# Kernel tuning notes

Hardware: AMD Instinct MI355X
Metric: run time of the kernel (lower is better)

## Reference

```python
import jax, jax.numpy as jnp
import numpy as np

K_SIM_SCHEDULE = [4, 8, 16]
K_CON_SCHEDULE = [2, 4, 8]
NEG = 1000000000.0


def _dual_adjacency(h, k_sim, k_con):
    """Binary causal dual adjacency (similar / dissimilar), no gradient."""
    B, T, D = h.shape
    h = jax.lax.stop_gradient(h)
    xn = h / jnp.maximum(jnp.linalg.norm(h, axis=-1, keepdims=True), 1e-12)
    sim = jnp.einsum('btd,bsd->bts', xn, xn)                 # (B,T,T)
    past = jnp.tril(jnp.ones((T, T), h.dtype), -1)           # strictly-past mask
    sim = sim * past - NEG * (1.0 - past)
    eff_sim = min(k_sim, T - 1)
    eff_con = min(k_con, max(0, T - 1 - eff_sim))
    bI = jnp.arange(B)[:, None, None]
    tI = jnp.arange(T)[None, :, None]
    A_sim = jnp.zeros((B, T, T), h.dtype)
    if eff_sim > 0:
        _, top_idx = jax.lax.top_k(sim, eff_sim)             # (B,T,k)
        A_sim = A_sim.at[bI, tI, top_idx].set(1.0) * past
    A_con = jnp.zeros((B, T, T), h.dtype)
    if eff_con > 0:
        sim_con = jnp.where(A_sim > 0, NEG, sim)
        _, bot_idx = jax.lax.top_k(-sim_con, eff_con)        # smallest eff_con
        A_con = A_con.at[bI, tI, bot_idx].set(1.0) * past * (1.0 - A_sim)
    return A_sim, A_con


def _aggregate(h, A):
    # unweighted mean over selected neighbors; empty rows -> zeros
    deg = jnp.sum(A, axis=-1, keepdims=True)
    return jnp.einsum('bts,bsd->btd', A, h) / jnp.maximum(deg, 1.0)


def setup_inputs() -> dict:
    key = jax.random.key(0)
    ks = jax.random.split(key, 2)
    B, T, D, R = 4, 2048, 512, 3
    x = jax.random.normal(ks[0], (B, T, D), dtype=jnp.float32)
    gain = jnp.ones((R, D), dtype=jnp.float32)
    bias = jnp.zeros((R, D), dtype=jnp.float32)
    log_mix = jnp.zeros((R,), dtype=jnp.float32)
    log_alpha = jnp.zeros((R,), dtype=jnp.float32)
    log_momentum = jnp.asarray(1.0, dtype=jnp.float32)
    log_scale = jnp.asarray(0.0, dtype=jnp.float32)
    return {"x": x, "gain": gain, "bias": bias, "log_mix": log_mix,
            "log_alpha": log_alpha, "log_momentum": log_momentum,
            "log_scale": log_scale}


def reference(x, gain, bias, log_mix, log_alpha, log_momentum, log_scale):
    momentum = jax.nn.sigmoid(log_momentum)
    scale = jax.nn.softplus(log_scale) + 0.01
    h = x
    for r in range(len(K_SIM_SCHEDULE)):
        mix = jax.nn.sigmoid(log_mix[r])
        alpha = jax.nn.sigmoid(log_alpha[r])
        A_sim, A_con = _dual_adjacency(h, K_SIM_SCHEDULE[r], K_CON_SCHEDULE[r])
        msg_pos = _aggregate(h, A_sim)
        msg_neg = _aggregate(h, A_con)
        ctx = alpha * msg_pos + (1.0 - alpha) * msg_neg
        blended = mix * h + (1.0 - mix) * ctx
        h_new = jax.nn.gelu(blended * gain[r] + bias[r], approximate=False)
        h = momentum * h + (1.0 - momentum) * h_new
    return (h - x) * scale
```

## Files before the change

### kernel.cpp

```cpp
#include <hip/hip_runtime.h>
#include <hip/hip_bf16.h>
#include <cstdint>
#include <cstddef>

#define BB 4
#define TT 2048
#define DD 512
#define NEG_INF (-3.402823466e+38f)
#define POS_INF (3.402823466e+38f)

typedef __attribute__((ext_vector_type(8))) short bf16x8;
typedef __attribute__((ext_vector_type(8))) unsigned short ushort8;
typedef __attribute__((ext_vector_type(4))) float f32x4;

__device__ __forceinline__ float sigmoidf_(float x){ return 1.0f/(1.0f+expf(-x)); }

__device__ __forceinline__ unsigned short f2bf(float x){
  __hip_bfloat16 b = __float2bfloat16(x);
  return *reinterpret_cast<unsigned short*>(&b);
}

__device__ __forceinline__ unsigned int fwd_map(float f){
  unsigned int b = __float_as_uint(f);
  return b ^ ((b & 0x80000000u) ? 0xFFFFFFFFu : 0x80000000u);
}
__device__ __forceinline__ float inv_map(unsigned int u){
  unsigned int b = (u & 0x80000000u) ? (u ^ 0x80000000u) : ~u;
  return __uint_as_float(b);
}

__device__ __forceinline__ unsigned long long shfl_xor64(unsigned long long x, int off){
  unsigned int hi = __shfl_xor((unsigned int)(x >> 32), off);
  unsigned int lo = __shfl_xor((unsigned int)x, off);
  return ((unsigned long long)hi << 32) | lo;
}

__global__ __launch_bounds__(64) void k_normsplit(const float* __restrict__ h, float* __restrict__ rnorm,
                                                  unsigned short* __restrict__ Xh, unsigned short* __restrict__ Xl){
  int row = blockIdx.x;
  const float* hr = h + (size_t)row*DD;
  int lane = threadIdx.x;
  float4 v0 = *(const float4*)&hr[lane*4];
  float4 v1 = *(const float4*)&hr[lane*4 + 256];
  float ss = v0.x*v0.x+v0.y*v0.y+v0.z*v0.z+v0.w*v0.w
           + v1.x*v1.x+v1.y*v1.y+v1.z*v1.z+v1.w*v1.w;
  #pragma unroll
  for (int off=32; off; off>>=1) ss += __shfl_xor(ss, off);
  float rn = 1.0f / fmaxf(sqrtf(ss), 1e-12f);
  if (lane==0) rnorm[row] = rn;

  float xs[8] = {v0.x,v0.y,v0.z,v0.w,v1.x,v1.y,v1.z,v1.w};
  unsigned short hb[8], lb[8];
  #pragma unroll
  for (int q=0;q<8;q++){
    float xn = xs[q]*rn;
    unsigned short hh = f2bf(xn);
    __hip_bfloat16 bh = *reinterpret_cast<__hip_bfloat16*>(&hh);
    float rem = xn - __bfloat162float(bh);
    hb[q] = hh; lb[q] = f2bf(rem);
  }
  ushort4 h0 = {hb[0],hb[1],hb[2],hb[3]}, h1 = {hb[4],hb[5],hb[6],hb[7]};
  ushort4 l0 = {lb[0],lb[1],lb[2],lb[3]}, l1 = {lb[4],lb[5],lb[6],lb[7]};
  *(ushort4*)&Xh[(size_t)row*DD + lane*4]       = h0;
  *(ushort4*)&Xh[(size_t)row*DD + lane*4 + 256] = h1;
  *(ushort4*)&Xl[(size_t)row*DD + lane*4]       = l0;
  *(ushort4*)&Xl[(size_t)row*DD + lane*4 + 256] = l1;
}

__global__ __launch_bounds__(256) void k_sim(const unsigned short* __restrict__ Xh,
                                             const unsigned short* __restrict__ Xl,
                                             float* __restrict__ sim, int b0){
  int p = blockIdx.x;
  int jt = (int)((sqrtf(8.0f*(float)p + 1.0f) - 1.0f)*0.5f);
  while ((jt+1)*(jt+2)/2 <= p) jt++;
  while (jt*(jt+1)/2 > p) jt--;
  int is = p - jt*(jt+1)/2;

  int bl = blockIdx.y;
  size_t xoff = (size_t)(b0 + bl)*TT*DD;
  const unsigned short* XhB = Xh + xoff;
  const unsigned short* XlB = Xl + xoff;
  float* simb = sim + (size_t)bl*TT*TT;
  int t0 = jt*128, s0 = is*128;

  __shared__ __align__(16) short As[128*32];
  __shared__ __align__(16) short Bs[128*32];

  int tid = threadIdx.x, wave = tid>>6, lane = tid&63;
  int wr = wave>>1, wc = wave&1;

  int srow = tid>>2;
  int sc8  = (tid&3)*8;

  f32x4 acc[4][4];
  #pragma unroll
  for (int m=0;m<4;m++)
    #pragma unroll
    for (int n=0;n<4;n++) acc[m][n] = (f32x4){0.f,0.f,0.f,0.f};

  ushort8 ra0, ra1, rb0, rb1;
  auto gload = [&](int s){
    int pass = s>>4; int kcol = (s&15)*32;
    const unsigned short* sA = (pass<2) ? XhB : XlB;
    const unsigned short* sB = (pass!=1) ? XhB : XlB;
    ra0 = *(const ushort8*)&sA[(size_t)(t0+srow)*DD + kcol + sc8];
    ra1 = *(const ushort8*)&sA[(size_t)(t0+srow+64)*DD + kcol + sc8];
    rb0 = *(const ushort8*)&sB[(size_t)(s0+srow)*DD + kcol + sc8];
    rb1 = *(const ushort8*)&sB[(size_t)(s0+srow+64)*DD + kcol + sc8];
  };

  gload(0);
  for (int s=0; s<48; ++s){
    __syncthreads();
    *(ushort8*)&As[srow*32 + sc8]      = ra0;
    *(ushort8*)&As[(srow+64)*32 + sc8] = ra1;
    *(ushort8*)&Bs[srow*32 + sc8]      = rb0;
    *(ushort8*)&Bs[(srow+64)*32 + sc8] = rb1;
    __syncthreads();
    if (s < 47) gload(s+1);

    int arow = wr*64 + (lane&15);
    int brow = wc*64 + (lane&15);
    int kb = (lane>>4)*8;
    bf16x8 af[4], bf[4];
    #pragma unroll
    for (int m=0;m<4;m++) af[m] = *(const bf16x8*)&As[(arow + m*16)*32 + kb];
    #pragma unroll
    for (int n=0;n<4;n++) bf[n] = *(const bf16x8*)&Bs[(brow + n*16)*32 + kb];
    #pragma unroll
    for (int m=0;m<4;m++)
      #pragma unroll
      for (int n=0;n<4;n++)
        acc[m][n] = __builtin_amdgcn_mfma_f32_16x16x32_bf16(af[m], bf[n], acc[m][n], 0, 0, 0);
  }

  #pragma unroll
  for (int m=0;m<4;m++){
    int t = t0 + wr*64 + m*16 + (lane>>4)*4;
    #pragma unroll
    for (int n=0;n<4;n++){
      int sc = s0 + wc*64 + n*16 + (lane&15);
      float* dst = simb + (size_t)t*TT + sc;
      #pragma unroll
      for (int j=0;j<4;j++) dst[(size_t)j*TT] = acc[m][n][j];
    }
  }
}

#define BMASK 0xFFFFFF00u
#define MKKEY(F,S) ((((unsigned long long)fwd_map(F)) << 32) | (unsigned int)(~(S)))
#define INS(KK) do{ unsigned long long a=(KK); \
  if (a > kv3){ \
    if (a > kv0){ unsigned long long tq=kv0; kv0=a; a=tq; } \
    if (a > kv1){ unsigned long long tq=kv1; kv1=a; a=tq; } \
    if (a > kv2){ unsigned long long tq=kv2; kv2=a; a=tq; } \
    kv3=a; } }while(0)

__device__ __forceinline__ unsigned int radix24(const float* __restrict__ srow, int t, int k1,
                                                unsigned int flip, int* sh, int lane){
  #pragma unroll
  for (int i=0;i<4;i++) sh[lane + i*64] = 0;
  int t4 = t & ~3;
  for (int s4 = lane*4; s4 < t4; s4 += 256){
    float4 f = *(const float4*)&srow[s4];
    unsigned int u0=fwd_map(f.x)^flip, u1=fwd_map(f.y)^flip, u2=fwd_map(f.z)^flip, u3=fwd_map(f.w)^flip;
    atomicAdd(&sh[u0>>24],1); atomicAdd(&sh[u1>>24],1);
    atomicAdd(&sh[u2>>24],1); atomicAdd(&sh[u3>>24],1);
  }
  for (int s = t4 + lane; s < t; s += 64){
    unsigned int u = fwd_map(srow[s])^flip;
    atomicAdd(&sh[u>>24],1);
  }
  unsigned int pfx = 0u; int kp = k1;
  #pragma unroll
  for (int pass = 0; pass < 3; ++pass){
    int shift = 24 - 8*pass;
    int m4 = sh[4*lane] + sh[4*lane+1] + sh[4*lane+2] + sh[4*lane+3];
    int x = __shfl(m4, 63-lane);
    #pragma unroll
    for (int off = 1; off < 64; off <<= 1){
      int v = __shfl_up(x, off);
      if (lane >= off) x += v;
    }
    int T = __shfl(x, 63-lane);
    int G = T - m4;
    bool hit = (G < kp) && (kp <= T);
    unsigned int npfx = 0u; int nkp = 0;
    if (hit){
      int c = G; int D = 4*lane;
      #pragma unroll
      for (int i = 3; i >= 0; --i){
        int hc = sh[4*lane + i];
        if (kp <= c + hc){ D = 4*lane + i; break; }
        c += hc;
      }
      npfx = pfx | ((unsigned int)D << shift);
      nkp = kp - c;
    }
    unsigned long long hm = __ballot(hit);
    int src = __ffsll(hm) - 1;
    pfx = __shfl(npfx, src);
    kp  = __shfl(nkp, src);
    if (pass == 2) break;

    int nshift = shift - 8;
    unsigned int keep = 0xFFFFFFFFu << shift;
    #pragma unroll
    for (int i=0;i<4;i++) sh[lane + i*64] = 0;
    for (int s4 = lane*4; s4 < t4; s4 += 256){
      float4 f = *(const float4*)&srow[s4];
      unsigned int u0=fwd_map(f.x)^flip, u1=fwd_map(f.y)^flip, u2=fwd_map(f.z)^flip, u3=fwd_map(f.w)^flip;
      if (((u0 ^ pfx) & keep) == 0) atomicAdd(&sh[(u0>>nshift)&255],1);
      if (((u1 ^ pfx) & keep) == 0) atomicAdd(&sh[(u1>>nshift)&255],1);
      if (((u2 ^ pfx) & keep) == 0) atomicAdd(&sh[(u2>>nshift)&255],1);
      if (((u3 ^ pfx) & keep) == 0) atomicAdd(&sh[(u3>>nshift)&255],1);
    }
    for (int s = t4 + lane; s < t; s += 64){
      unsigned int u = fwd_map(srow[s])^flip;
      if (((u ^ pfx) & keep) == 0) atomicAdd(&sh[(u>>nshift)&255],1);
    }
  }
  return pfx;
}

template<int ESIM, int ECON>
__global__ __launch_bounds__(256) void k_topk(const float* __restrict__ sim, int b0,
                                              const float* __restrict__ h, const float* __restrict__ rnorm,
                                              int* __restrict__ topidx, int* __restrict__ botidx,
                                              int* __restrict__ bcnt){
  constexpr int K1  = ESIM + 8;
  constexpr int K1B = ESIM + ECON + 8;
  constexpr int CANDCAP = 40;
  constexpr int EQCAP = 44;
  constexpr float TAU = 5e-5f;
  __shared__ int s_hist[4][256];
  __shared__ int s_cand[4][CANDCAP];
  __shared__ int s_eq[4][EQCAP];
  __shared__ int s_sel[4][ESIM];
  __shared__ int s_bot[4][16];
  __shared__ int s_cnt[4][2];

  int tid = threadIdx.x, lane = tid & 63, wid = tid >> 6;
  int lrow = blockIdx.x*4 + wid;
  int bl = lrow >> 11, t = lrow & (TT-1);
  int gb = b0 + bl;
  int grow = (gb << 11) | t;

  if (t <= ESIM){
    if (lane < t) topidx[(size_t)grow*16 + lane] = lane;
    if (lane == 0) bcnt[grow] = 0;
    return;
  }
  const float* srow = sim + (size_t)lrow*TT;
  const float* hb  = h + (size_t)gb*TT*DD;
  const float* rnb = rnorm + (size_t)gb*TT;

  int* sh    = s_hist[wid];
  int* scand = s_cand[wid];
  int* seq   = s_eq[wid];
  int* ssel  = s_sel[wid];
  int* sbot  = s_bot[wid];
  int t4 = t & ~3;

  unsigned long long kv0=0, kv1=0, kv2=0, kv3=0;
  {
    int s4 = lane*4;
    for (; s4 + 772 <= t4; s4 += 1024){
      float4 f0 = *(const float4*)&srow[s4];
      float4 f1 = *(const float4*)&srow[s4+256];
      float4 f2 = *(const float4*)&srow[s4+512];
      float4 f3 = *(const float4*)&srow[s4+768];
      INS(MKKEY(f0.x,s4));     INS(MKKEY(f0.y,s4+1));   INS(MKKEY(f0.z,s4+2));   INS(MKKEY(f0.w,s4+3));
      INS(MKKEY(f1.x,s4+256)); INS(MKKEY(f1.y,s4+257)); INS(MKKEY(f1.z,s4+258)); INS(MKKEY(f1.w,s4+259));
      INS(MKKEY(f2.x,s4+512)); INS(MKKEY(f2.y,s4+513)); INS(MKKEY(f2.z,s4+514)); INS(MKKEY(f2.w,s4+515));
      INS(MKKEY(f3.x,s4+768)); INS(MKKEY(f3.y,s4+769)); INS(MKKEY(f3.z,s4+770)); INS(MKKEY(f3.w,s4+771));
    }
    for (; s4 < t4; s4 += 256){
      float4 f = *(const float4*)&srow[s4];
      INS(MKKEY(f.x,s4)); INS(MKKEY(f.y,s4+1)); INS(MKKEY(f.z,s4+2)); INS(MKKEY(f.w,s4+3));
    }
    for (int s = t4 + lane; s < t; s += 64) INS(MKKEY(srow[s],s));
  }

  unsigned long long cert = kv3;
  #pragma unroll
  for (int off=32; off; off>>=1){
    unsigned long long oc = shfl_xor64(cert, off);
    if (oc > cert) cert = oc;
  }

  int myidx = 0x7fffffff;
  float vA = 0.f, vB = 0.f;
  unsigned long long keyLast = 0ull;
  #pragma unroll
  for (int k = 0; k <= ESIM; ++k){
    unsigned long long bk = kv0;
    #pragma unroll
    for (int off=32; off; off>>=1){
      unsigned long long ok = shfl_xor64(bk, off);
      if (ok > bk) bk = ok;
    }
    if (kv0 == bk){ kv0=kv1; kv1=kv2; kv2=kv3; kv3=0ull; }
    if (lane == k) myidx = (int)(~(unsigned int)bk);
    if (k == ESIM-1) vA = inv_map((unsigned int)(bk >> 32));
    if (k == ESIM){ vB = inv_map((unsigned int)(bk >> 32)); keyLast = bk; }
  }

  bool fb = (cert > keyLast) || (vA - vB < TAU);
  if (!fb){
    if (lane < ESIM){
      ssel[lane] = myidx;
      topidx[(size_t)grow*16 + lane] = myidx;
    }
  } else {
    int k1 = min(t, K1);
    unsigned int thr = radix24(srow, t, k1, 0u, sh, lane);

    if (lane == 0){ s_cnt[wid][0] = 0; s_cnt[wid][1] = 0; }
    for (int s4 = lane*4; s4 < t4; s4 += 256){
      float4 f = *(const float4*)&srow[s4];
      unsigned int uu[4] = {fwd_map(f.x), fwd_map(f.y), fwd_map(f.z), fwd_map(f.w)};
      #pragma unroll
      for (int q=0;q<4;q++){
        unsigned int b24 = uu[q] & BMASK;
        if (b24 > thr){ int p = atomicAdd(&s_cnt[wid][0],1); if (p < CANDCAP) scand[p] = s4+q; }
        else if (b24 == thr){ int p = atomicAdd(&s_cnt[wid][1],1); if (p < EQCAP) seq[p] = s4+q; }
      }
    }
    for (int s = t4 + lane; s < t; s += 64){
      unsigned int b24 = fwd_map(srow[s]) & BMASK;
      if (b24 > thr){ int p = atomicAdd(&s_cnt[wid][0],1); if (p < CANDCAP) scand[p] = s; }
      else if (b24 == thr){ int p = atomicAdd(&s_cnt[wid][1],1); if (p < EQCAP) seq[p] = s; }
    }
    int c_gt = min(s_cnt[wid][0], CANDCAP);
    int c_eq = min(s_cnt[wid][1], EQCAP);
    int ncand = min(c_gt + c_eq, 64);

    unsigned int myu = 0u; int myi = 0x7fffffff;
    if (lane < ncand){
      myi = (lane < c_gt) ? scand[lane] : seq[lane - c_gt];
      myu = fwd_map(srow[myi]);
    }

    float fvA = 0.f, fvB = 0.f;
    {
      unsigned int cu = myu; int ci = myi;
      #pragma unroll
      for (int k = 0; k <= ESIM; ++k){
        unsigned int bu = cu; int bi = ci;
        #pragma unroll
        for (int off=32; off; off>>=1){
          unsigned int ou = __shfl_xor(bu, off); int oi = __shfl_xor(bi, off);
          if (ou > bu || (ou == bu && oi < bi)){ bu = ou; bi = oi; }
        }
        if (k < ESIM && lane == 0) ssel[k] = bi;
        if (k == ESIM-1) fvA = inv_map(bu);
        if (k == ESIM)   fvB = inv_map(bu);
        if (ci == bi){ cu = 0u; ci = 0x7fffffff; }
      }
    }

    bool resc = (fvA - fvB < TAU);
    if (resc){
      const float* hq = hb + (size_t)t*DD;
      float rt = rnb[t];
      float4 q0 = *(const float4*)&hq[lane*4];
      float4 q1 = *(const float4*)&hq[lane*4 + 256];
      float ev = NEG_INF;
      for (int j = 0; j < ncand; ++j){
        int idx = (j < c_gt) ? scand[j] : seq[j - c_gt];
        const float* hc = hb + (size_t)idx*DD;
        float4 c0 = *(const float4*)&hc[lane*4];
        float4 c1 = *(const float4*)&hc[lane*4 + 256];
        float pp = q0.x*c0.x+q0.y*c0.y+q0.z*c0.z+q0.w*c0.w
                 + q1.x*c1.x+q1.y*c1.y+q1.z*c1.z+q1.w*c1.w;
        #pragma unroll
        for (int off=32; off; off>>=1) pp += __shfl_xor(pp, off);
        float ex = pp * rt * rnb[idx];
        if (lane == j) ev = ex;
      }
      float rv = (lane < ncand) ? ev : NEG_INF;
      int   ri = myi;
      #pragma unroll
      for (int k = 0; k < ESIM; ++k){
        float bv = rv; int bi = ri;
        #pragma unroll
        for (int off=32; off; off>>=1){
          float ov = __shfl_xor(bv, off); int oi = __shfl_xor(bi, off);
          if (ov > bv || (ov == bv && oi < bi)){ bv = ov; bi = oi; }
        }
        if (lane == 0) ssel[k] = bi;
        if (ri == bi) rv = NEG_INF;
      }
    }
    if (lane < ESIM) topidx[(size_t)grow*16 + lane] = ssel[lane];
  }

  int need = ECON - (TT - t);
  int cnt2 = 0;
  if (need > 0){
    constexpr unsigned int FLIP = 0xFFFFFFFFu;
    int k1b = min(t, K1B);
    unsigned int thrb = radix24(srow, t, k1b, FLIP, sh, lane);

    if (lane == 0){ s_cnt[wid][0] = 0; s_cnt[wid][1] = 0; }
    for (int s4 = lane*4; s4 < t4; s4 += 256){
      float4 f = *(const float4*)&srow[s4];
      unsigned int uu[4] = {fwd_map(f.x)^FLIP, fwd_map(f.y)^FLIP, fwd_map(f.z)^FLIP, fwd_map(f.w)^FLIP};
      #pragma unroll
      for (int q=0;q<4;q++){
        unsigned int b24 = uu[q] & BMASK;
        if (b24 > thrb){ int p = atomicAdd(&s_cnt[wid][0],1); if (p < CANDCAP) scand[p] = s4+q; }
        else if (b24 == thrb){ int p = atomicAdd(&s_cnt[wid][1],1); if (p < EQCAP) seq[p] = s4+q; }
      }
    }
    for (int s = t4 + lane; s < t; s += 64){
      unsigned int u = fwd_map(srow[s])^FLIP;
      unsigned int b24 = u & BMASK;
      if (b24 > thrb){ int p = atomicAdd(&s_cnt[wid][0],1); if (p < CANDCAP) scand[p] = s; }
      else if (b24 == thrb){ int p = atomicAdd(&s_cnt[wid][1],1); if (p < EQCAP) seq[p] = s; }
    }
    int bc_gt = min(s_cnt[wid][0], CANDCAP);
    int bc_eq = min(s_cnt[wid][1], EQCAP);
    int ncb = min(bc_gt + bc_eq, 64);

    unsigned int mu = 0u; int mi = 0x7fffffff;
    if (lane < ncb){
      mi = (lane < bc_gt) ? scand[lane] : seq[lane - bc_gt];
      mu = fwd_map(srow[mi]) ^ FLIP;
    }
    float wA = 0.f, wB = 0.f;
    unsigned int cu = mu; int ci = mi;
    #pragma unroll
    for (int k = 0; k < K1B; ++k){
      if (k < ncb && cnt2 < need + 8){
        unsigned int bu = cu; int bi = ci;
        #pragma unroll
        for (int off=32; off; off>>=1){
          unsigned int ou = __shfl_xor(bu, off); int oi = __shfl_xor(bi, off);
          if (ou > bu || (ou == bu && oi < bi)){ bu = ou; bi = oi; }
        }
        if (ci == bi){ cu = 0u; ci = 0x7fffffff; }
        bool mem = false;
        #pragma unroll
        for (int j=0;j<ESIM;j++) if (ssel[j] == bi) mem = true;
        if (!mem){
          if (lane == 0) sbot[cnt2] = bi;
          float val = inv_map(bu ^ FLIP);
          if (cnt2 == need-1) wA = val;
          if (cnt2 == need)   wB = val;
          cnt2++;
        }
      }
    }
    int npick = min(need, cnt2);
    bool rb = (cnt2 > need) && (wB - wA < TAU);
    if (!rb){
      if (lane < npick) botidx[(size_t)grow*8 + lane] = sbot[lane];
    } else {
      const float* hq = hb + (size_t)t*DD;
      float rt = rnb[t];
      float4 q0 = *(const float4*)&hq[lane*4];
      float4 q1 = *(const float4*)&hq[lane*4 + 256];
      float ev = POS_INF; int ei = 0x7fffffff;
      for (int j = 0; j < cnt2; ++j){
        int idx = sbot[j];
        const float* hc = hb + (size_t)idx*DD;
        float4 c0 = *(const float4*)&hc[lane*4];
        float4 c1 = *(const float4*)&hc[lane*4 + 256];
        float pp = q0.x*c0.x+q0.y*c0.y+q0.z*c0.z+q0.w*c0.w
                 + q1.x*c1.x+q1.y*c1.y+q1.z*c1.z+q1.w*c1.w;
        #pragma unroll
        for (int off=32; off; off>>=1) pp += __shfl_xor(pp, off);
        float ex = pp * rt * rnb[idx];
        if (lane == j){ ev = ex; ei = idx; }
      }
      #pragma unroll
      for (int k = 0; k < ECON; ++k){
        if (k < npick){
          float bv = ev; int bi = ei;
          #pragma unroll
          for (int off=32; off; off>>=1){
            float ov = __shfl_xor(bv, off); int oi = __shfl_xor(bi, off);
            if (ov < bv || (ov == bv && oi < bi)){ bv = ov; bi = oi; }
          }
          if (lane == 0) botidx[(size_t)grow*8 + k] = bi;
          if (ei == bi) ev = POS_INF;
        }
      }
    }
    cnt2 = npick;
  }
  if (lane == 0) bcnt[grow] = cnt2;
}

__global__ __launch_bounds__(256) void k_agg(const float* __restrict__ hsrc, float* __restrict__ hdst,
                                             const int* __restrict__ topidx, const int* __restrict__ botidx,
                                             const int* __restrict__ bcnt,
                                             const float* __restrict__ gain, const float* __restrict__ bias,
                                             const float* __restrict__ log_mix, const float* __restrict__ log_alpha,
                                             const float* __restrict__ log_momentum, int r, int eff_sim){
  int row = blockIdx.x;
  int b = row >> 11; int t = row & (TT-1);
  int n_sim = min(eff_sim, t);
  int n_con = bcnt[row];
  float mix      = sigmoidf_(log_mix[r]);
  float alpha    = sigmoidf_(log_alpha[r]);
  float momentum = sigmoidf_(log_momentum[0]);
  const float* hb = hsrc + (size_t)b*TT*DD;

  __shared__ int sidx[16];
  __shared__ int scidx[8];
  if (threadIdx.x < 16) sidx[threadIdx.x]  = (threadIdx.x < n_sim) ? topidx[(size_t)row*16 + threadIdx.x] : 0;
  if (threadIdx.x < 8)  scidx[threadIdx.x] = (threadIdx.x < n_con) ? botidx[(size_t)row*8  + threadIdx.x] : 0;
  __syncthreads();

  #pragma unroll
  for (int e = threadIdx.x; e < DD; e += 256){
    float sp = 0.f;
    for (int j=0;j<n_sim;j++) sp += hb[(size_t)sidx[j]*DD + e];
    float sn = 0.f;
    for (int j=0;j<n_con;j++) sn += hb[(size_t)scidx[j]*DD + e];
    float mp = sp / (float)max(n_sim, 1);
    float mn = sn / (float)max(n_con, 1);
    float ctx = alpha*mp + (1.f-alpha)*mn;
    float hv = hsrc[(size_t)row*DD + e];
    float blended = mix*hv + (1.f-mix)*ctx;
    float u = blended*gain[e] + bias[e];
    float g = 0.5f*u*(1.0f + erff(u*0.7071067811865475f));
    hdst[(size_t)row*DD + e] = momentum*hv + (1.f-momentum)*g;
  }
}

__global__ __launch_bounds__(256) void k_final(const float* __restrict__ hfin, const float* __restrict__ x,
                                               const float* __restrict__ log_scale, float* __restrict__ out, int n){
  float scale = log1pf(expf(log_scale[0])) + 0.01f;
  int i = blockIdx.x*256 + threadIdx.x;
  if (i < n) out[i] = (hfin[i] - x[i]) * scale;
}

extern "C" void kernel_launch(void* const* d_in, const int* in_sizes, int n_in,
                              void* d_out, int out_size, void* d_ws, size_t ws_size,
                              hipStream_t stream) {
  const float* x         = (const float*)d_in[0];
  const float* gain      = (const float*)d_in[1];
  const float* bias      = (const float*)d_in[2];
  const float* log_mix   = (const float*)d_in[3];
  const float* log_alpha = (const float*)d_in[4];
  const float* log_mom   = (const float*)d_in[5];
  const float* log_scale = (const float*)d_in[6];

  float* hA = (float*)d_out;
  char* ws = (char*)d_ws;
  size_t off = 0;
  auto alloc = [&](size_t bytes){ void* p = ws + off; off += (bytes + 255) & ~(size_t)255; return p; };

  float*          hB     = (float*)alloc((size_t)BB*TT*DD*4);
  float*          rnorm  = (float*)alloc((size_t)BB*TT*4);
  int*            topidx = (int*)  alloc((size_t)BB*TT*16*4);
  int*            botidx = (int*)  alloc((size_t)BB*TT*8*4);
  int*            bcnt   = (int*)  alloc((size_t)BB*TT*4);
  unsigned short* Xh     = (unsigned short*)alloc((size_t)BB*TT*DD*2);
  unsigned short* Xl     = (unsigned short*)alloc((size_t)BB*TT*DD*2);

  size_t rem = (ws_size > off) ? (ws_size - off) : 0;
  int cb = (int)(rem / ((size_t)TT*TT*4));
  if (cb < 1) cb = 1;
  if (cb > BB) cb = BB;
  float* sim = (float*)alloc((size_t)cb*TT*TT*4);

  const float* hsrc = x;
  float* hdst = hB;
  const int ks[3] = {4, 8, 16};

  for (int r = 0; r < 3; ++r){
    k_normsplit<<<BB*TT, 64, 0, stream>>>(hsrc, rnorm, Xh, Xl);
    for (int b0 = 0; b0 < BB; b0 += cb){
      int nb = (BB - b0 < cb) ? (BB - b0) : cb;
      dim3 g(136, nb);
      k_sim<<<g, 256, 0, stream>>>(Xh, Xl, sim, b0);
      if (r == 0)      k_topk<4,2><<<nb*TT/4, 256, 0, stream>>>(sim, b0, hsrc, rnorm, topidx, botidx, bcnt);
      else if (r == 1) k_topk<8,4><<<nb*TT/4, 256, 0, stream>>>(sim, b0, hsrc, rnorm, topidx, botidx, bcnt);
      else             k_topk<16,8><<<nb*TT/4, 256, 0, stream>>>(sim, b0, hsrc, rnorm, topidx, botidx, bcnt);
    }
    k_agg<<<BB*TT, 256, 0, stream>>>(hsrc, hdst, topidx, botidx, bcnt,
                                     gain + (size_t)r*DD, bias + (size_t)r*DD,
                                     log_mix, log_alpha, log_mom, r, ks[r]);
    if (r == 0){ hsrc = hB; hdst = hA; }
    else if (r == 1){ hsrc = hA; hdst = hB; }
  }
  k_final<<<(BB*TT*DD)/256, 256, 0, stream>>>(hB, x, log_scale, (float*)d_out, BB*TT*DD);
}
```

Measured before the change: 462.4 us.

## Process four top-k rows per wavefront with interleaved streaming scans

Each wavefront in the top-k kernel now handles four rows spread a quarter of the row range apart, instead of one. The first streaming top-4 scan of all four rows runs up front with independent loads interleaved, to expose more memory-level parallelism and balance the triangular causal workload. The radix fallback is marked noinline to limit code growth. The cost is a quarter as many blocks, more registers for sixteen 64-bit key slots, and predicated loads that may read past t, though those reads stay within the row.

```diff
diff --git a/kernel.cpp b/kernel.cpp
--- a/kernel.cpp
+++ b/kernel.cpp
@@ -148,16 +148,38 @@
 }
 
 #define BMASK 0xFFFFFF00u
-#define MKKEY(F,S) ((((unsigned long long)fwd_map(F)) << 32) | (unsigned int)(~(S)))
-#define INS(KK) do{ unsigned long long a=(KK); \
-  if (a > kv3){ \
-    if (a > kv0){ unsigned long long tq=kv0; kv0=a; a=tq; } \
-    if (a > kv1){ unsigned long long tq=kv1; kv1=a; a=tq; } \
-    if (a > kv2){ unsigned long long tq=kv2; kv2=a; a=tq; } \
-    kv3=a; } }while(0)
-
-__device__ __forceinline__ unsigned int radix24(const float* __restrict__ srow, int t, int k1,
-                                                unsigned int flip, int* sh, int lane){
+#define MK64(F,S) ((((unsigned long long)fwd_map(F)) << 32) | (unsigned int)(~(S)))
+#define INS4(K0,K1v,K2,K3,KK) do{ unsigned long long a_=(KK); \
+  if (a_ > K3){ \
+    if (a_ > K0){ unsigned long long q_=K0; K0=a_; a_=q_; } \
+    if (a_ > K1v){ unsigned long long q_=K1v; K1v=a_; a_=q_; } \
+    if (a_ > K2){ unsigned long long q_=K2; K2=a_; a_=q_; } \
+    K3=a_; } }while(0)
+
+#define SWROW(BASE, PTR, TX, Q0,Q1,Q2,Q3) do{ \
+  float4 f0_=*(const float4*)&(PTR)[(BASE)],     f1_=*(const float4*)&(PTR)[(BASE)+256], \
+         f2_=*(const float4*)&(PTR)[(BASE)+512], f3_=*(const float4*)&(PTR)[(BASE)+768]; \
+  int sb_=(BASE); \
+  if(sb_    <(TX)) INS4(Q0,Q1,Q2,Q3, MK64(f0_.x,sb_));     \
+  if(sb_+1  <(TX)) INS4(Q0,Q1,Q2,Q3, MK64(f0_.y,sb_+1));   \
+  if(sb_+2  <(TX)) INS4(Q0,Q1,Q2,Q3, MK64(f0_.z,sb_+2));   \
+  if(sb_+3  <(TX)) INS4(Q0,Q1,Q2,Q3, MK64(f0_.w,sb_+3));   \
+  if(sb_+256<(TX)) INS4(Q0,Q1,Q2,Q3, MK64(f1_.x,sb_+256)); \
+  if(sb_+257<(TX)) INS4(Q0,Q1,Q2,Q3, MK64(f1_.y,sb_+257)); \
+  if(sb_+258<(TX)) INS4(Q0,Q1,Q2,Q3, MK64(f1_.z,sb_+258)); \
+  if(sb_+259<(TX)) INS4(Q0,Q1,Q2,Q3, MK64(f1_.w,sb_+259)); \
+  if(sb_+512<(TX)) INS4(Q0,Q1,Q2,Q3, MK64(f2_.x,sb_+512)); \
+  if(sb_+513<(TX)) INS4(Q0,Q1,Q2,Q3, MK64(f2_.y,sb_+513)); \
+  if(sb_+514<(TX)) INS4(Q0,Q1,Q2,Q3, MK64(f2_.z,sb_+514)); \
+  if(sb_+515<(TX)) INS4(Q0,Q1,Q2,Q3, MK64(f2_.w,sb_+515)); \
+  if(sb_+768<(TX)) INS4(Q0,Q1,Q2,Q3, MK64(f3_.x,sb_+768)); \
+  if(sb_+769<(TX)) INS4(Q0,Q1,Q2,Q3, MK64(f3_.y,sb_+769)); \
+  if(sb_+770<(TX)) INS4(Q0,Q1,Q2,Q3, MK64(f3_.z,sb_+770)); \
+  if(sb_+771<(TX)) INS4(Q0,Q1,Q2,Q3, MK64(f3_.w,sb_+771)); \
+}while(0)
+
+__device__ __attribute__((noinline)) unsigned int radix24(const float* __restrict__ srow, int t, int k1,
+                                                          unsigned int flip, int* sh, int lane){
   #pragma unroll
   for (int i=0;i<4;i++) sh[lane + i*64] = 0;
   int t4 = t & ~3;
@@ -227,7 +249,7 @@
 __global__ __launch_bounds__(256) void k_topk(const float* __restrict__ sim, int b0,
                                               const float* __restrict__ h, const float* __restrict__ rnorm,
                                               int* __restrict__ topidx, int* __restrict__ botidx,
-                                              int* __restrict__ bcnt){
+                                              int* __restrict__ bcnt, int rquarter){
   constexpr int K1  = ESIM + 8;
   constexpr int K1B = ESIM + ECON + 8;
   constexpr int CANDCAP = 40;
@@ -241,257 +263,267 @@
   __shared__ int s_cnt[4][2];
 
   int tid = threadIdx.x, lane = tid & 63, wid = tid >> 6;
-  int lrow = blockIdx.x*4 + wid;
-  int bl = lrow >> 11, t = lrow & (TT-1);
-  int gb = b0 + bl;
-  int grow = (gb << 11) | t;
-
-  if (t <= ESIM){
-    if (lane < t) topidx[(size_t)grow*16 + lane] = lane;
-    if (lane == 0) bcnt[grow] = 0;
-    return;
-  }
-  const float* srow = sim + (size_t)lrow*TT;
-  const float* hb  = h + (size_t)gb*TT*DD;
-  const float* rnb = rnorm + (size_t)gb*TT;
+  int W = blockIdx.x*4 + wid;
+
+  int lr0 = W, lr1 = W + rquarter, lr2 = W + 2*rquarter, lr3 = W + 3*rquarter;
+  int tA = lr0 & (TT-1), tB = lr1 & (TT-1), tC = lr2 & (TT-1), tD = lr3 & (TT-1);
+  const float* sA_ = sim + (size_t)lr0*TT;
+  const float* sB_ = sim + (size_t)lr1*TT;
+  const float* sC_ = sim + (size_t)lr2*TT;
+  const float* sD_ = sim + (size_t)lr3*TT;
 
   int* sh    = s_hist[wid];
   int* scand = s_cand[wid];
   int* seq   = s_eq[wid];
   int* ssel  = s_sel[wid];
   int* sbot  = s_bot[wid];
-  int t4 = t & ~3;
-
-  unsigned long long kv0=0, kv1=0, kv2=0, kv3=0;
+
+  unsigned long long kA0=0,kA1=0,kA2=0,kA3=0, kB0=0,kB1=0,kB2=0,kB3=0,
+                     kC0=0,kC1=0,kC2=0,kC3=0, kD0=0,kD1=0,kD2=0,kD3=0;
   {
-    int s4 = lane*4;
-    for (; s4 + 772 <= t4; s4 += 1024){
-      float4 f0 = *(const float4*)&srow[s4];
-      float4 f1 = *(const float4*)&srow[s4+256];
-      float4 f2 = *(const float4*)&srow[s4+512];
-      float4 f3 = *(const float4*)&srow[s4+768];
-      INS(MKKEY(f0.x,s4));     INS(MKKEY(f0.y,s4+1));   INS(MKKEY(f0.z,s4+2));   INS(MKKEY(f0.w,s4+3));
-      INS(MKKEY(f1.x,s4+256)); INS(MKKEY(f1.y,s4+257)); INS(MKKEY(f1.z,s4+258)); INS(MKKEY(f1.w,s4+259));
-      INS(MKKEY(f2.x,s4+512)); INS(MKKEY(f2.y,s4+513)); INS(MKKEY(f2.z,s4+514)); INS(MKKEY(f2.w,s4+515));
-      INS(MKKEY(f3.x,s4+768)); INS(MKKEY(f3.y,s4+769)); INS(MKKEY(f3.z,s4+770)); INS(MKKEY(f3.w,s4+771));
-    }
-    for (; s4 < t4; s4 += 256){
-      float4 f = *(const float4*)&srow[s4];
-      INS(MKKEY(f.x,s4)); INS(MKKEY(f.y,s4+1)); INS(MKKEY(f.z,s4+2)); INS(MKKEY(f.w,s4+3));
-    }
-    for (int s = t4 + lane; s < t; s += 64) INS(MKKEY(srow[s],s));
-  }
-
-  unsigned long long cert = kv3;
-  #pragma unroll
-  for (int off=32; off; off>>=1){
-    unsigned long long oc = shfl_xor64(cert, off);
-    if (oc > cert) cert = oc;
-  }
-
-  int myidx = 0x7fffffff;
-  float vA = 0.f, vB = 0.f;
-  unsigned long long keyLast = 0ull;
-  #pragma unroll
-  for (int k = 0; k <= ESIM; ++k){
-    unsigned long long bk = kv0;
+    int base0 = lane*4;
+    if (tA > ESIM) SWROW(base0, sA_, tA, kA0,kA1,kA2,kA3);
+    if (tB > ESIM) SWROW(base0, sB_, tB, kB0,kB1,kB2,kB3);
+    if (tC > ESIM) SWROW(base0, sC_, tC, kC0,kC1,kC2,kC3);
+    if (tD > ESIM) SWROW(base0, sD_, tD, kD0,kD1,kD2,kD3);
+    int base1 = 1024 + lane*4;
+    if (tA > 1024) SWROW(base1, sA_, tA, kA0,kA1,kA2,kA3);
+    if (tB > 1024) SWROW(base1, sB_, tB, kB0,kB1,kB2,kB3);
+    if (tC > 1024) SWROW(base1, sC_, tC, kC0,kC1,kC2,kC3);
+    if (tD > 1024) SWROW(base1, sD_, tD, kD0,kD1,kD2,kD3);
+  }
+
+  #pragma unroll
+  for (int q = 0; q < 4; ++q){
+    unsigned long long w0,w1,w2,w3;
+    const float* srow; int t, lrow;
+    if (q==0){ w0=kA0;w1=kA1;w2=kA2;w3=kA3; srow=sA_; t=tA; lrow=lr0; }
+    else if (q==1){ w0=kB0;w1=kB1;w2=kB2;w3=kB3; srow=sB_; t=tB; lrow=lr1; }
+    else if (q==2){ w0=kC0;w1=kC1;w2=kC2;w3=kC3; srow=sC_; t=tC; lrow=lr2; }
+    else { w0=kD0;w1=kD1;w2=kD2;w3=kD3; srow=sD_; t=tD; lrow=lr3; }
+    int gb = b0 + (lrow >> 11);
+    int grow = (gb << 11) | t;
+    const float* hb  = h + (size_t)gb*TT*DD;
+    const float* rnb = rnorm + (size_t)gb*TT;
+    int t4 = t & ~3;
+
+    if (t <= ESIM){
+      if (lane < t) topidx[(size_t)grow*16 + lane] = lane;
+      if (lane == 0) bcnt[grow] = 0;
+      continue;
+    }
+
+    unsigned long long cert = w3;
     #pragma unroll
     for (int off=32; off; off>>=1){
-      unsigned long long ok = shfl_xor64(bk, off);
-      if (ok > bk) bk = ok;
-    }
-    if (kv0 == bk){ kv0=kv1; kv1=kv2; kv2=kv3; kv3=0ull; }
-    if (lane == k) myidx = (int)(~(unsigned int)bk);
-    if (k == ESIM-1) vA = inv_map((unsigned int)(bk >> 32));
-    if (k == ESIM){ vB = inv_map((unsigned int)(bk >> 32)); keyLast = bk; }
-  }
-
-  bool fb = (cert > keyLast) || (vA - vB < TAU);
-  if (!fb){
-    if (lane < ESIM){
-      ssel[lane] = myidx;
-      topidx[(size_t)grow*16 + lane] = myidx;
-    }
-  } else {
-    int k1 = min(t, K1);
-    unsigned int thr = radix24(srow, t, k1, 0u, sh, lane);
-
-    if (lane == 0){ s_cnt[wid][0] = 0; s_cnt[wid][1] = 0; }
-    for (int s4 = lane*4; s4 < t4; s4 += 256){
-      float4 f = *(const float4*)&srow[s4];
-      unsigned int uu[4] = {fwd_map(f.x), fwd_map(f.y), fwd_map(f.z), fwd_map(f.w)};
+      unsigned long long oc = shfl_xor64(cert, off);
+      if (oc > cert) cert = oc;
+    }
+
+    int myidx = 0x7fffffff;
+    float vA = 0.f, vB = 0.f;
+    unsigned long long keyLast = 0ull;
+    #pragma unroll
+    for (int k = 0; k <= ESIM; ++k){
+      unsigned long long bk = w0;
       #pragma unroll
-      for (int q=0;q<4;q++){
-        unsigned int b24 = uu[q] & BMASK;
-        if (b24 > thr){ int p = atomicAdd(&s_cnt[wid][0],1); if (p < CANDCAP) scand[p] = s4+q; }
-        else if (b24 == thr){ int p = atomicAdd(&s_cnt[wid][1],1); if (p < EQCAP) seq[p] = s4+q; }
-      }
-    }
-    for (int s = t4 + lane; s < t; s += 64){
-      unsigned int b24 = fwd_map(srow[s]) & BMASK;
-      if (b24 > thr){ int p = atomicAdd(&s_cnt[wid][0],1); if (p < CANDCAP) scand[p] = s; }
-      else if (b24 == thr){ int p = atomicAdd(&s_cnt[wid][1],1); if (p < EQCAP) seq[p] = s; }
-    }
-    int c_gt = min(s_cnt[wid][0], CANDCAP);
-    int c_eq = min(s_cnt[wid][1], EQCAP);
-    int ncand = min(c_gt + c_eq, 64);
-
-    unsigned int myu = 0u; int myi = 0x7fffffff;
-    if (lane < ncand){
-      myi = (lane < c_gt) ? scand[lane] : seq[lane - c_gt];
-      myu = fwd_map(srow[myi]);
-    }
-
-    float fvA = 0.f, fvB = 0.f;
-    {
-      unsigned int cu = myu; int ci = myi;
-      #pragma unroll
-      for (int k = 0; k <= ESIM; ++k){
-        unsigned int bu = cu; int bi = ci;
+      for (int off=32; off; off>>=1){
+        unsigned long long ok = shfl_xor64(bk, off);
+        if (ok > bk) bk = ok;
+      }
+      if (w0 == bk){ w0=w1; w1=w2; w2=w3; w3=0ull; }
+      if (lane == k) myidx = (int)(~(unsigned int)bk);
+      if (k == ESIM-1) vA = inv_map((unsigned int)(bk >> 32));
+      if (k == ESIM){ vB = inv_map((unsigned int)(bk >> 32)); keyLast = bk; }
+    }
+
+    bool fb = (cert > keyLast) || (vA - vB < TAU);
+    if (!fb){
+      if (lane < ESIM){
+        ssel[lane] = myidx;
+        topidx[(size_t)grow*16 + lane] = myidx;
+      }
+    } else {
+      int k1 = min(t, K1);
+      unsigned int thr = radix24(srow, t, k1, 0u, sh, lane);
+
+      if (lane == 0){ s_cnt[wid][0] = 0; s_cnt[wid][1] = 0; }
+      for (int s4 = lane*4; s4 < t4; s4 += 256){
+        float4 f = *(const float4*)&srow[s4];
+        unsigned int uu[4] = {fwd_map(f.x), fwd_map(f.y), fwd_map(f.z), fwd_map(f.w)};
         #pragma unroll
-        for (int off=32; off; off>>=1){
-          unsigned int ou = __shfl_xor(bu, off); int oi = __shfl_xor(bi, off);
-          if (ou > bu || (ou == bu && oi < bi)){ bu = ou; bi = oi; }
-        }
-        if (k < ESIM && lane == 0) ssel[k] = bi;
-        if (k == ESIM-1) fvA = inv_map(bu);
-        if (k == ESIM)   fvB = inv_map(bu);
-        if (ci == bi){ cu = 0u; ci = 0x7fffffff; }
-      }
-    }
-
-    bool resc = (fvA - fvB < TAU);
-    if (resc){
-      const float* hq = hb + (size_t)t*DD;
-      float rt = rnb[t];
-      float4 q0 = *(const float4*)&hq[lane*4];
-      float4 q1 = *(const float4*)&hq[lane*4 + 256];
-      float ev = NEG_INF;
-      for (int j = 0; j < ncand; ++j){
-        int idx = (j < c_gt) ? scand[j] : seq[j - c_gt];
-        const float* hc = hb + (size_t)idx*DD;
-        float4 c0 = *(const float4*)&hc[lane*4];
-        float4 c1 = *(const float4*)&hc[lane*4 + 256];
-        float pp = q0.x*c0.x+q0.y*c0.y+q0.z*c0.z+q0.w*c0.w
-                 + q1.x*c1.x+q1.y*c1.y+q1.z*c1.z+q1.w*c1.w;
+        for (int qq=0;qq<4;qq++){
+          unsigned int b24 = uu[qq] & BMASK;
+          if (b24 > thr){ int p = atomicAdd(&s_cnt[wid][0],1); if (p < CANDCAP) scand[p] = s4+qq; }
+          else if (b24 == thr){ int p = atomicAdd(&s_cnt[wid][1],1); if (p < EQCAP) seq[p] = s4+qq; }
+        }
+      }
+      for (int s = t4 + lane; s < t; s += 64){
+        unsigned int b24 = fwd_map(srow[s]) & BMASK;
+        if (b24 > thr){ int p = atomicAdd(&s_cnt[wid][0],1); if (p < CANDCAP) scand[p] = s; }
+        else if (b24 == thr){ int p = atomicAdd(&s_cnt[wid][1],1); if (p < EQCAP) seq[p] = s; }
+      }
+      int c_gt = min(s_cnt[wid][0], CANDCAP);
+      int c_eq = min(s_cnt[wid][1], EQCAP);
+      int ncand = min(c_gt + c_eq, 64);
+
+      unsigned int myu = 0u; int myi = 0x7fffffff;
+      if (lane < ncand){
+        myi = (lane < c_gt) ? scand[lane] : seq[lane - c_gt];
+        myu = fwd_map(srow[myi]);
+      }
+
+      float fvA = 0.f, fvB = 0.f;
+      {
+        unsigned int cu = myu; int ci = myi;
         #pragma unroll
-        for (int off=32; off; off>>=1) pp += __shfl_xor(pp, off);
-        float ex = pp * rt * rnb[idx];
-        if (lane == j) ev = ex;
-      }
-      float rv = (lane < ncand) ? ev : NEG_INF;
-      int   ri = myi;
-      #pragma unroll
-      for (int k = 0; k < ESIM; ++k){
-        float bv = rv; int bi = ri;
+        for (int k = 0; k <= ESIM; ++k){
+          unsigned int bu = cu; int bi = ci;
+          #pragma unroll
+          for (int off=32; off; off>>=1){
+            unsigned int ou = __shfl_xor(bu, off); int oi = __shfl_xor(bi, off);
+            if (ou > bu || (ou == bu && oi < bi)){ bu = ou; bi = oi; }
+          }
+          if (k < ESIM && lane == 0) ssel[k] = bi;
+          if (k == ESIM-1) fvA = inv_map(bu);
+          if (k == ESIM)   fvB = inv_map(bu);
+          if (ci == bi){ cu = 0u; ci = 0x7fffffff; }
+        }
+      }
+
+      bool resc = (fvA - fvB < TAU);
+      if (resc){
+        const float* hq = hb + (size_t)t*DD;
+        float rt = rnb[t];
+        float4 q0 = *(const float4*)&hq[lane*4];
+        float4 q1 = *(const float4*)&hq[lane*4 + 256];
+        float ev = NEG_INF;
+        for (int j = 0; j < ncand; ++j){
+          int idx = (j < c_gt) ? scand[j] : seq[j - c_gt];
+          const float* hc = hb + (size_t)idx*DD;
+          float4 c0 = *(const float4*)&hc[lane*4];
+          float4 c1 = *(const float4*)&hc[lane*4 + 256];
+          float pp = q0.x*c0.x+q0.y*c0.y+q0.z*c0.z+q0.w*c0.w
+                   + q1.x*c1.x+q1.y*c1.y+q1.z*c1.z+q1.w*c1.w;
+          #pragma unroll
+          for (int off=32; off; off>>=1) pp += __shfl_xor(pp, off);
+          float ex = pp * rt * rnb[idx];
+          if (lane == j) ev = ex;
+        }
+        float rv = (lane < ncand) ? ev : NEG_INF;
+        int   ri = myi;
         #pragma unroll
-        for (int off=32; off; off>>=1){
-          float ov = __shfl_xor(bv, off); int oi = __shfl_xor(bi, off);
-          if (ov > bv || (ov == bv && oi < bi)){ bv = ov; bi = oi; }
-        }
-        if (lane == 0) ssel[k] = bi;
-        if (ri == bi) rv = NEG_INF;
-      }
-    }
-    if (lane < ESIM) topidx[(size_t)grow*16 + lane] = ssel[lane];
-  }
-
-  int need = ECON - (TT - t);
-  int cnt2 = 0;
-  if (need > 0){
-    constexpr unsigned int FLIP = 0xFFFFFFFFu;
-    int k1b = min(t, K1B);
-    unsigned int thrb = radix24(srow, t, k1b, FLIP, sh, lane);
-
-    if (lane == 0){ s_cnt[wid][0] = 0; s_cnt[wid][1] = 0; }
-    for (int s4 = lane*4; s4 < t4; s4 += 256){
-      float4 f = *(const float4*)&srow[s4];
-      unsigned int uu[4] = {fwd_map(f.x)^FLIP, fwd_map(f.y)^FLIP, fwd_map(f.z)^FLIP, fwd_map(f.w)^FLIP};
-      #pragma unroll
-      for (int q=0;q<4;q++){
-        unsigned int b24 = uu[q] & BMASK;
-        if (b24 > thrb){ int p = atomicAdd(&s_cnt[wid][0],1); if (p < CANDCAP) scand[p] = s4+q; }
-        else if (b24 == thrb){ int p = atomicAdd(&s_cnt[wid][1],1); if (p < EQCAP) seq[p] = s4+q; }
-      }
-    }
-    for (int s = t4 + lane; s < t; s += 64){
-      unsigned int u = fwd_map(srow[s])^FLIP;
-      unsigned int b24 = u & BMASK;
-      if (b24 > thrb){ int p = atomicAdd(&s_cnt[wid][0],1); if (p < CANDCAP) scand[p] = s; }
-      else if (b24 == thrb){ int p = atomicAdd(&s_cnt[wid][1],1); if (p < EQCAP) seq[p] = s; }
-    }
-    int bc_gt = min(s_cnt[wid][0], CANDCAP);
-    int bc_eq = min(s_cnt[wid][1], EQCAP);
-    int ncb = min(bc_gt + bc_eq, 64);
-
-    unsigned int mu = 0u; int mi = 0x7fffffff;
-    if (lane < ncb){
-      mi = (lane < bc_gt) ? scand[lane] : seq[lane - bc_gt];
-      mu = fwd_map(srow[mi]) ^ FLIP;
-    }
-    float wA = 0.f, wB = 0.f;
-    unsigned int cu = mu; int ci = mi;
-    #pragma unroll
-    for (int k = 0; k < K1B; ++k){
-      if (k < ncb && cnt2 < need + 8){
-        unsigned int bu = cu; int bi = ci;
-        #pragma unroll
-        for (int off=32; off; off>>=1){
-          unsigned int ou = __shfl_xor(bu, off); int oi = __shfl_xor(bi, off);
-          if (ou > bu || (ou == bu && oi < bi)){ bu = ou; bi = oi; }
-        }
-        if (ci == bi){ cu = 0u; ci = 0x7fffffff; }
-        bool mem = false;
-        #pragma unroll
-        for (int j=0;j<ESIM;j++) if (ssel[j] == bi) mem = true;
-        if (!mem){
-          if (lane == 0) sbot[cnt2] = bi;
-          float val = inv_map(bu ^ FLIP);
-          if (cnt2 == need-1) wA = val;
-          if (cnt2 == need)   wB = val;
-          cnt2++;
-        }
-      }
-    }
-    int npick = min(need, cnt2);
-    bool rb = (cnt2 > need) && (wB - wA < TAU);
-    if (!rb){
-      if (lane < npick) botidx[(size_t)grow*8 + lane] = sbot[lane];
-    } else {
-      const float* hq = hb + (size_t)t*DD;
-      float rt = rnb[t];
-      float4 q0 = *(const float4*)&hq[lane*4];
-      float4 q1 = *(const float4*)&hq[lane*4 + 256];
-      float ev = POS_INF; int ei = 0x7fffffff;
-      for (int j = 0; j < cnt2; ++j){
-        int idx = sbot[j];
-        const float* hc = hb + (size_t)idx*DD;
-        float4 c0 = *(const float4*)&hc[lane*4];
-        float4 c1 = *(const float4*)&hc[lane*4 + 256];
-        float pp = q0.x*c0.x+q0.y*c0.y+q0.z*c0.z+q0.w*c0.w
-                 + q1.x*c1.x+q1.y*c1.y+q1.z*c1.z+q1.w*c1.w;
-        #pragma unroll
-        for (int off=32; off; off>>=1) pp += __shfl_xor(pp, off);
-        float ex = pp * rt * rnb[idx];
-        if (lane == j){ ev = ex; ei = idx; }
-      }
-      #pragma unroll
-      for (int k = 0; k < ECON; ++k){
-        if (k < npick){
-          float bv = ev; int bi = ei;
+        for (int k = 0; k < ESIM; ++k){
+          float bv = rv; int bi = ri;
           #pragma unroll
           for (int off=32; off; off>>=1){
             float ov = __shfl_xor(bv, off); int oi = __shfl_xor(bi, off);
-            if (ov < bv || (ov == bv && oi < bi)){ bv = ov; bi = oi; }
+            if (ov > bv || (ov == bv && oi < bi)){ bv = ov; bi = oi; }
           }
-          if (lane == 0) botidx[(size_t)grow*8 + k] = bi;
-          if (ei == bi) ev = POS_INF;
-        }
-      }
-    }
-    cnt2 = npick;
-  }
-  if (lane == 0) bcnt[grow] = cnt2;
+          if (lane == 0) ssel[k] = bi;
+          if (ri == bi) rv = NEG_INF;
+        }
+      }
+      if (lane < ESIM) topidx[(size_t)grow*16 + lane] = ssel[lane];
+    }
+
+    int need = ECON - (TT - t);
+    int cnt2 = 0;
+    if (need > 0){
+      constexpr unsigned int FLIP = 0xFFFFFFFFu;
+      int k1b = min(t, K1B);
+      unsigned int thrb = radix24(srow, t, k1b, FLIP, sh, lane);
+
+      if (lane == 0){ s_cnt[wid][0] = 0; s_cnt[wid][1] = 0; }
+      for (int s4 = lane*4; s4 < t4; s4 += 256){
+        float4 f = *(const float4*)&srow[s4];
+        unsigned int uu[4] = {fwd_map(f.x)^FLIP, fwd_map(f.y)^FLIP, fwd_map(f.z)^FLIP, fwd_map(f.w)^FLIP};
+        #pragma unroll
+        for (int qq=0;qq<4;qq++){
+          unsigned int b24 = uu[qq] & BMASK;
+          if (b24 > thrb){ int p = atomicAdd(&s_cnt[wid][0],1); if (p < CANDCAP) scand[p] = s4+qq; }
+          else if (b24 == thrb){ int p = atomicAdd(&s_cnt[wid][1],1); if (p < EQCAP) seq[p] = s4+qq; }
+        }
+      }
+      for (int s = t4 + lane; s < t; s += 64){
+        unsigned int u = fwd_map(srow[s])^FLIP;
+        unsigned int b24 = u & BMASK;
+        if (b24 > thrb){ int p = atomicAdd(&s_cnt[wid][0],1); if (p < CANDCAP) scand[p] = s; }
+        else if (b24 == thrb){ int p = atomicAdd(&s_cnt[wid][1],1); if (p < EQCAP) seq[p] = s; }
+      }
+      int bc_gt = min(s_cnt[wid][0], CANDCAP);
+      int bc_eq = min(s_cnt[wid][1], EQCAP);
+      int ncb = min(bc_gt + bc_eq, 64);
+
+      unsigned int mu = 0u; int mi = 0x7fffffff;
+      if (lane < ncb){
+        mi = (lane < bc_gt) ? scand[lane] : seq[lane - bc_gt];
+        mu = fwd_map(srow[mi]) ^ FLIP;
+      }
+      float wA = 0.f, wB = 0.f;
+      unsigned int cu = mu; int ci = mi;
+      #pragma unroll
+      for (int k = 0; k < K1B; ++k){
+        if (k < ncb && cnt2 < need + 8){
+          unsigned int bu = cu; int bi = ci;
+          #pragma unroll
+          for (int off=32; off; off>>=1){
+            unsigned int ou = __shfl_xor(bu, off); int oi = __shfl_xor(bi, off);
+            if (ou > bu || (ou == bu && oi < bi)){ bu = ou; bi = oi; }
+          }
+          if (ci == bi){ cu = 0u; ci = 0x7fffffff; }
+          bool mem = false;
+          #pragma unroll
+          for (int j=0;j<ESIM;j++) if (ssel[j] == bi) mem = true;
+          if (!mem){
+            if (lane == 0) sbot[cnt2] = bi;
+            float val = inv_map(bu ^ FLIP);
+            if (cnt2 == need-1) wA = val;
+            if (cnt2 == need)   wB = val;
+            cnt2++;
+          }
+        }
+      }
+      int npick = min(need, cnt2);
+      bool rb = (cnt2 > need) && (wB - wA < TAU);
+      if (!rb){
+        if (lane < npick) botidx[(size_t)grow*8 + lane] = sbot[lane];
+      } else {
+        const float* hq = hb + (size_t)t*DD;
+        float rt = rnb[t];
+        float4 q0 = *(const float4*)&hq[lane*4];
+        float4 q1 = *(const float4*)&hq[lane*4 + 256];
+        float ev = POS_INF; int ei = 0x7fffffff;
+        for (int j = 0; j < cnt2; ++j){
+          int idx = sbot[j];
+          const float* hc = hb + (size_t)idx*DD;
+          float4 c0 = *(const float4*)&hc[lane*4];
+          float4 c1 = *(const float4*)&hc[lane*4 + 256];
+          float pp = q0.x*c0.x+q0.y*c0.y+q0.z*c0.z+q0.w*c0.w
+                   + q1.x*c1.x+q1.y*c1.y+q1.z*c1.z+q1.w*c1.w;
+          #pragma unroll
+          for (int off=32; off; off>>=1) pp += __shfl_xor(pp, off);
+          float ex = pp * rt * rnb[idx];
+          if (lane == j){ ev = ex; ei = idx; }
+        }
+        #pragma unroll
+        for (int k = 0; k < ECON; ++k){
+          if (k < npick){
+            float bv = ev; int bi = ei;
+            #pragma unroll
+            for (int off=32; off; off>>=1){
+              float ov = __shfl_xor(bv, off); int oi = __shfl_xor(bi, off);
+              if (ov < bv || (ov == bv && oi < bi)){ bv = ov; bi = oi; }
+            }
+            if (lane == 0) botidx[(size_t)grow*8 + k] = bi;
+            if (ei == bi) ev = POS_INF;
+          }
+        }
+      }
+      cnt2 = npick;
+    }
+    if (lane == 0) bcnt[grow] = cnt2;
+  }
 }
 
 __global__ __launch_bounds__(256) void k_agg(const float* __restrict__ hsrc, float* __restrict__ hdst,
@@ -579,9 +611,10 @@
       int nb = (BB - b0 < cb) ? (BB - b0) : cb;
       dim3 g(136, nb);
       k_sim<<<g, 256, 0, stream>>>(Xh, Xl, sim, b0);
-      if (r == 0)      k_topk<4,2><<<nb*TT/4, 256, 0, stream>>>(sim, b0, hsrc, rnorm, topidx, botidx, bcnt);
-      else if (r == 1) k_topk<8,4><<<nb*TT/4, 256, 0, stream>>>(sim, b0, hsrc, rnorm, topidx, botidx, bcnt);
-      else             k_topk<16,8><<<nb*TT/4, 256, 0, stream>>>(sim, b0, hsrc, rnorm, topidx, botidx, bcnt);
+      int rq = nb*TT/4;
+      if (r == 0)      k_topk<4,2><<<nb*TT/16, 256, 0, stream>>>(sim, b0, hsrc, rnorm, topidx, botidx, bcnt, rq);
+      else if (r == 1) k_topk<8,4><<<nb*TT/16, 256, 0, stream>>>(sim, b0, hsrc, rnorm, topidx, botidx, bcnt, rq);
+      else             k_topk<16,8><<<nb*TT/16, 256, 0, stream>>>(sim, b0, hsrc, rnorm, topidx, botidx, bcnt, rq);
     }
     k_agg<<<BB*TT, 256, 0, stream>>>(hsrc, hdst, topidx, botidx, bcnt,
                                      gain + (size_t)r*DD, bias + (size_t)r*DD,
```

New measurement: 741.6 us. +60.4%, slower.

## Double-buffer k_sim tiles via direct global-to-LDS loads with 512 threads

Applied to the files above, without the earlier changes.

The similarity GEMM kernel now loads A/B tiles straight into LDS with global_load_lds instead of staging through registers. It double-buffers those tiles so the next k-step's load overlaps the current MFMA work, which also cuts the loop to one barrier per step. Block size doubles to 8 waves, each computing a 64x32 subtile, which lowers per-wave accumulator registers. The risks are the ordering and visibility of async LDS writes around the single barrier, since the LDS layout relies on the per-wave 512-element chunk placement of the intrinsic.

```diff
diff --git a/kernel.cpp b/kernel.cpp
--- a/kernel.cpp
+++ b/kernel.cpp
@@ -33,6 +33,12 @@
   unsigned int hi = __shfl_xor((unsigned int)(x >> 32), off);
   unsigned int lo = __shfl_xor((unsigned int)x, off);
   return ((unsigned long long)hi << 32) | lo;
+}
+
+__device__ __forceinline__ void gl_lds16(const unsigned short* g, short* l){
+  __builtin_amdgcn_global_load_lds(
+    (const __attribute__((address_space(1))) unsigned int*)g,
+    (__attribute__((address_space(3))) unsigned int*)l, 16, 0, 0);
 }
 
 __global__ __launch_bounds__(64) void k_normsplit(const float* __restrict__ h, float* __restrict__ rnorm,
@@ -67,7 +73,7 @@
   *(ushort4*)&Xl[(size_t)row*DD + lane*4 + 256] = l1;
 }
 
-__global__ __launch_bounds__(256) void k_sim(const unsigned short* __restrict__ Xh,
+__global__ __launch_bounds__(512) void k_sim(const unsigned short* __restrict__ Xh,
                                              const unsigned short* __restrict__ Xl,
                                              float* __restrict__ sim, int b0){
   int p = blockIdx.x;
@@ -83,63 +89,61 @@
   float* simb = sim + (size_t)bl*TT*TT;
   int t0 = jt*128, s0 = is*128;
 
-  __shared__ __align__(16) short As[128*32];
-  __shared__ __align__(16) short Bs[128*32];
+  __shared__ __align__(16) short As[2][4096];
+  __shared__ __align__(16) short Bs[2][4096];
 
   int tid = threadIdx.x, wave = tid>>6, lane = tid&63;
-  int wr = wave>>1, wc = wave&1;
+  int wr = wave>>2, wc = wave&3;
 
   int srow = tid>>2;
   int sc8  = (tid&3)*8;
 
-  f32x4 acc[4][4];
+  size_t offA = (size_t)(t0 + srow)*DD + sc8;
+  size_t offB = (size_t)(s0 + srow)*DD + sc8;
+
+  f32x4 acc[4][2];
   #pragma unroll
   for (int m=0;m<4;m++)
     #pragma unroll
-    for (int n=0;n<4;n++) acc[m][n] = (f32x4){0.f,0.f,0.f,0.f};
-
-  ushort8 ra0, ra1, rb0, rb1;
-  auto gload = [&](int s){
+    for (int n=0;n<2;n++) acc[m][n] = (f32x4){0.f,0.f,0.f,0.f};
+
+  auto stage = [&](int s, int buf){
     int pass = s>>4; int kcol = (s&15)*32;
     const unsigned short* sA = (pass<2) ? XhB : XlB;
     const unsigned short* sB = (pass!=1) ? XhB : XlB;
-    ra0 = *(const ushort8*)&sA[(size_t)(t0+srow)*DD + kcol + sc8];
-    ra1 = *(const ushort8*)&sA[(size_t)(t0+srow+64)*DD + kcol + sc8];
-    rb0 = *(const ushort8*)&sB[(size_t)(s0+srow)*DD + kcol + sc8];
-    rb1 = *(const ushort8*)&sB[(size_t)(s0+srow+64)*DD + kcol + sc8];
+    gl_lds16(sA + offA + kcol, &As[buf][wave*512]);
+    gl_lds16(sB + offB + kcol, &Bs[buf][wave*512]);
   };
 
-  gload(0);
+  stage(0, 0);
+  __syncthreads();
+
+  int arow = wr*64 + (lane&15);
+  int brow = wc*32 + (lane&15);
+  int kb = (lane>>4)*8;
+
   for (int s=0; s<48; ++s){
+    int cur = s & 1;
+    if (s < 47) stage(s+1, cur^1);
+    bf16x8 af[4], bf[2];
+    #pragma unroll
+    for (int m=0;m<4;m++) af[m] = *(const bf16x8*)&As[cur][(arow + m*16)*32 + kb];
+    #pragma unroll
+    for (int n=0;n<2;n++) bf[n] = *(const bf16x8*)&Bs[cur][(brow + n*16)*32 + kb];
+    #pragma unroll
+    for (int m=0;m<4;m++)
+      #pragma unroll
+      for (int n=0;n<2;n++)
+        acc[m][n] = __builtin_amdgcn_mfma_f32_16x16x32_bf16(af[m], bf[n], acc[m][n], 0, 0, 0);
     __syncthreads();
-    *(ushort8*)&As[srow*32 + sc8]      = ra0;
-    *(ushort8*)&As[(srow+64)*32 + sc8] = ra1;
-    *(ushort8*)&Bs[srow*32 + sc8]      = rb0;
-    *(ushort8*)&Bs[(srow+64)*32 + sc8] = rb1;
-    __syncthreads();
-    if (s < 47) gload(s+1);
-
-    int arow = wr*64 + (lane&15);
-    int brow = wc*64 + (lane&15);
-    int kb = (lane>>4)*8;
-    bf16x8 af[4], bf[4];
-    #pragma unroll
-    for (int m=0;m<4;m++) af[m] = *(const bf16x8*)&As[(arow + m*16)*32 + kb];
-    #pragma unroll
-    for (int n=0;n<4;n++) bf[n] = *(const bf16x8*)&Bs[(brow + n*16)*32 + kb];
-    #pragma unroll
-    for (int m=0;m<4;m++)
-      #pragma unroll
-      for (int n=0;n<4;n++)
-        acc[m][n] = __builtin_amdgcn_mfma_f32_16x16x32_bf16(af[m], bf[n], acc[m][n], 0, 0, 0);
   }
 
   #pragma unroll
   for (int m=0;m<4;m++){
     int t = t0 + wr*64 + m*16 + (lane>>4)*4;
     #pragma unroll
-    for (int n=0;n<4;n++){
-      int sc = s0 + wc*64 + n*16 + (lane&15);
+    for (int n=0;n<2;n++){
+      int sc = s0 + wc*32 + n*16 + (lane&15);
       float* dst = simb + (size_t)t*TT + sc;
       #pragma unroll
       for (int j=0;j<4;j++) dst[(size_t)j*TT] = acc[m][n][j];
@@ -578,7 +582,7 @@
     for (int b0 = 0; b0 < BB; b0 += cb){
       int nb = (BB - b0 < cb) ? (BB - b0) : cb;
       dim3 g(136, nb);
-      k_sim<<<g, 256, 0, stream>>>(Xh, Xl, sim, b0);
+      k_sim<<<g, 512, 0, stream>>>(Xh, Xl, sim, b0);
       if (r == 0)      k_topk<4,2><<<nb*TT/4, 256, 0, stream>>>(sim, b0, hsrc, rnorm, topidx, botidx, bcnt);
       else if (r == 1) k_topk<8,4><<<nb*TT/4, 256, 0, stream>>>(sim, b0, hsrc, rnorm, topidx, botidx, bcnt);
       else             k_topk<16,8><<<nb*TT/4, 256, 0, stream>>>(sim, b0, hsrc, rnorm, topidx, botidx, bcnt);
```

Result: no change. 454.0 us (-1.8%).
